# Kernel tuning notes

Hardware: AMD Instinct MI355X
Metric: run time of the kernel (lower is better)

The kernel has to match this reference:

```python
import jax, jax.numpy as jnp
import numpy as np

M = 255   # filter_order
P = 80    # frame_period


def setup_inputs() -> dict:
    key = jax.random.key(0)
    k1, k2 = jax.random.split(key)
    B, N = 8, 800
    T = N * P
    x = jax.random.normal(k1, (B, T), dtype=jnp.float32)
    h = jax.random.normal(k2, (B, N, M + 1), dtype=jnp.float32)
    return {"x": x, "h": h}


def _zerodf(x, h):
    # x: (B, T) excitation; h: (B, N, M+1) per-frame FIR coefficients, T = N*P
    B, T = x.shape
    N = h.shape[1]
    # left-pad with M zeros, then sliding windows of length M+1, stride 1
    x_pad = jnp.pad(x, ((0, 0), (M, 0)))                       # (B, T+M)
    idx = jnp.arange(T)[:, None] + jnp.arange(M + 1)[None, :]  # (T, M+1)
    xw = x_pad[:, idx]                                         # (B, T, M+1); window t = [x[t-M], ..., x[t]]
    # flip coeffs so xw . h_flip = sum_m h_m[t] * x[t-m]
    hf = h[..., ::-1]                                          # (B, N, M+1)
    # linear interpolation of coeffs from frame rate to sample rate,
    # holding the last frame (replicate pad): w[n*P+k] = lerp(h[n], h[n+1], k/P)
    hp = jnp.concatenate([hf, hf[:, -1:, :]], axis=1)          # (B, N+1, M+1)
    frac = (jnp.arange(P, dtype=x.dtype) / P)[None, None, :, None]  # (1,1,P,1)
    hi = hp[:, :-1, None, :] * (1.0 - frac) + hp[:, 1:, None, :] * frac  # (B,N,P,M+1)
    hi = hi.reshape(B, N * P, M + 1)                           # (B, T, M+1)
    return jnp.sum(xw * hi, axis=-1)                           # (B, T)


def reference(x, h):
    return _zerodf(x, h)
```

## Files before the change

### kernel.cpp

```cpp
#include <hip/hip_runtime.h>


#define TAPS 256
#define PP 80
#define BB 8
#define NN 800
#define TT (NN * PP)
#define FPB 8
#define TPF 16
#define RR 5
#define NTHREADS (FPB * TPF)
#define HSTRIDE 260
#define XWIN (FPB * PP + TAPS - 1)
#define CHUNKS (NN / FPB)

__global__ __launch_bounds__(NTHREADS) void azdf_kernel(
    const float* __restrict__ x, const float* __restrict__ h,
    float* __restrict__ out)
{
    __shared__ float sh[(FPB + 1) * HSTRIDE];
    __shared__ float sx[XWIN + 1];

    const int tid = threadIdx.x;
    const int blk = blockIdx.x;
    const int b   = blk / CHUNKS;
    const int nc  = blk % CHUNKS;
    const int n0  = nc * FPB;
    const int t0  = n0 * PP;

    const float* hb = h + (size_t)b * NN * TAPS;
    for (int i4 = tid; i4 < (FPB + 1) * (TAPS / 4); i4 += NTHREADS) {
        int r  = i4 >> 6;
        int k4 = i4 & 63;
        int gr = n0 + r;
        if (gr > NN - 1) gr = NN - 1;
        float4 v = ((const float4*)(hb + (size_t)gr * TAPS))[k4];
        ((float4*)(sh + r * HSTRIDE))[k4] = v;
    }

    const float* xb = x + (size_t)b * TT;
    for (int i = tid; i < XWIN; i += NTHREADS) {
        int g = t0 - (TAPS - 1) + i;
        sx[i] = (g >= 0) ? xb[g] : 0.0f;
    }
    __syncthreads();

    const int lf   = tid / TPF;
    const int lane = tid % TPF;
    const int p0   = lane * RR;
    const float* h0 = sh + lf * HSTRIDE;
    const float* h1 = h0 + HSTRIDE;
    const int base = lf * PP + p0 + (TAPS - 1);

    float acc0[RR], acc1[RR];
    #pragma unroll
    for (int r = 0; r < RR; ++r) { acc0[r] = 0.0f; acc1[r] = 0.0f; }

    for (int k = 0; k < TAPS; k += 4) {
        float xv[RR + 3];
        #pragma unroll
        for (int j = 0; j < RR + 3; ++j) xv[j] = sx[base - k - 3 + j];
        #pragma unroll
        for (int d = 0; d < 4; ++d) {
            float c0 = h0[k + d];
            float c1 = h1[k + d];
            #pragma unroll
            for (int r = 0; r < RR; ++r) {
                float xr = xv[r + 3 - d];
                acc0[r] = fmaf(xr, c0, acc0[r]);
                acc1[r] = fmaf(xr, c1, acc1[r]);
            }
        }
    }

    float* ob = out + (size_t)b * TT + t0 + lf * PP + p0;
    #pragma unroll
    for (int r = 0; r < RR; ++r) {
        float f = (float)(p0 + r) * (1.0f / PP);
        ob[r] = acc0[r] + f * (acc1[r] - acc0[r]);
    }
}

extern "C" void kernel_launch(void* const* d_in, const int* in_sizes, int n_in,
                              void* d_out, int out_size, void* d_ws, size_t ws_size,
                              hipStream_t stream) {
    const float* x = (const float*)d_in[0];
    const float* h = (const float*)d_in[1];
    float* out    = (float*)d_out;
    azdf_kernel<<<BB * CHUNKS, NTHREADS, 0, stream>>>(x, h, out);
}
```

Measured before the change: 71.50 us.

## Use float4 shared loads with sliding register window and larger frame tiles

Each block now covers 16 frames with 320 threads, and each thread computes 4 consecutive outputs instead of 5, so output addresses line up with float4 stores. The inner loop keeps an 8-element register window of x that it shifts every 4 taps, and it prefetches the next float4 of coefficients. This replaces the scalar LDS reads with vectorized ones. Blocks get more LDS and threads but there are half as many of them, which may reduce the number of waves and the occupancy balance.

```diff
diff --git a/kernel.cpp b/kernel.cpp
--- a/kernel.cpp
+++ b/kernel.cpp
@@ -6,12 +6,13 @@
 #define BB 8
 #define NN 800
 #define TT (NN * PP)
-#define FPB 8
-#define TPF 16
-#define RR 5
+#define FPB 16
+#define TPF 20
+#define RR 4
 #define NTHREADS (FPB * TPF)
 #define HSTRIDE 260
-#define XWIN (FPB * PP + TAPS - 1)
+#define XB 260
+#define XLEN (FPB * PP + XB + 4)
 #define CHUNKS (NN / FPB)
 
 __global__ __launch_bounds__(NTHREADS) void azdf_kernel(
@@ -19,7 +20,7 @@
     float* __restrict__ out)
 {
     __shared__ float sh[(FPB + 1) * HSTRIDE];
-    __shared__ float sx[XWIN + 1];
+    __shared__ float sx[XLEN];
 
     const int tid = threadIdx.x;
     const int blk = blockIdx.x;
@@ -29,56 +30,71 @@
     const int t0  = n0 * PP;
 
     const float* hb = h + (size_t)b * NN * TAPS;
-    for (int i4 = tid; i4 < (FPB + 1) * (TAPS / 4); i4 += NTHREADS) {
-        int r  = i4 >> 6;
-        int k4 = i4 & 63;
+    for (int i = tid; i < (FPB + 1) * (TAPS / 4); i += NTHREADS) {
+        int r  = i >> 6;
+        int q  = i & 63;
         int gr = n0 + r;
         if (gr > NN - 1) gr = NN - 1;
-        float4 v = ((const float4*)(hb + (size_t)gr * TAPS))[k4];
-        ((float4*)(sh + r * HSTRIDE))[k4] = v;
+        float4 v = ((const float4*)(hb + (size_t)gr * TAPS))[q];
+        ((float4*)(sh + r * HSTRIDE))[q] = v;
     }
 
     const float* xb = x + (size_t)b * TT;
-    for (int i = tid; i < XWIN; i += NTHREADS) {
-        int g = t0 - (TAPS - 1) + i;
-        sx[i] = (g >= 0) ? xb[g] : 0.0f;
+    for (int i = tid; i < XLEN; i += NTHREADS) {
+        int g = t0 + i - XB;
+        sx[i] = (g >= 0 && g < TT) ? xb[g] : 0.0f;
     }
     __syncthreads();
 
-    const int lf   = tid / TPF;
-    const int lane = tid % TPF;
-    const int p0   = lane * RR;
-    const float* h0 = sh + lf * HSTRIDE;
-    const float* h1 = h0 + HSTRIDE;
-    const int base = lf * PP + p0 + (TAPS - 1);
+    const int lf    = tid / TPF;
+    const int p0    = (tid % TPF) * RR;
+    const int xbase = XB + 4 * tid;
+    const float* hA = sh + lf * HSTRIDE;
+    const float* hB = hA + HSTRIDE;
 
     float acc0[RR], acc1[RR];
     #pragma unroll
     for (int r = 0; r < RR; ++r) { acc0[r] = 0.0f; acc1[r] = 0.0f; }
 
+    float W[8];
+    *(float4*)&W[0] = *(const float4*)&sx[xbase - 4];
+    *(float4*)&W[4] = *(const float4*)&sx[xbase];
+
+    float4 c0 = *(const float4*)hA;
+    float4 c1 = *(const float4*)hB;
+
+    #pragma unroll 4
     for (int k = 0; k < TAPS; k += 4) {
-        float xv[RR + 3];
-        #pragma unroll
-        for (int j = 0; j < RR + 3; ++j) xv[j] = sx[base - k - 3 + j];
+        float4 u0 = c0, u1 = c1;
+        c0 = *(const float4*)(hA + k + 4);
+        c1 = *(const float4*)(hB + k + 4);
+        float4 xn = *(const float4*)&sx[xbase - k - 8];
+
+        const float* u0f = (const float*)&u0;
+        const float* u1f = (const float*)&u1;
         #pragma unroll
         for (int d = 0; d < 4; ++d) {
-            float c0 = h0[k + d];
-            float c1 = h1[k + d];
+            float cc0 = u0f[d];
+            float cc1 = u1f[d];
             #pragma unroll
             for (int r = 0; r < RR; ++r) {
-                float xr = xv[r + 3 - d];
-                acc0[r] = fmaf(xr, c0, acc0[r]);
-                acc1[r] = fmaf(xr, c1, acc1[r]);
+                float xr = W[r - d + 4];
+                acc0[r] = fmaf(xr, cc0, acc0[r]);
+                acc1[r] = fmaf(xr, cc1, acc1[r]);
             }
         }
+        W[4] = W[0]; W[5] = W[1]; W[6] = W[2]; W[7] = W[3];
+        *(float4*)&W[0] = xn;
     }
 
-    float* ob = out + (size_t)b * TT + t0 + lf * PP + p0;
+    float4 o;
+    float* of = (float*)&o;
     #pragma unroll
     for (int r = 0; r < RR; ++r) {
         float f = (float)(p0 + r) * (1.0f / PP);
-        ob[r] = acc0[r] + f * (acc1[r] - acc0[r]);
+        of[r] = acc0[r] + f * (acc1[r] - acc0[r]);
     }
+    *(float4*)(out + (size_t)b * TT + t0 + 4 * tid) = o;
 }
 
 extern "C" void kernel_launch(void* const* d_in, const int* in_sizes, int n_in,
```

Result: slower. 74.02 us (+3.5%).
